# Kernel optimization log

Hardware: AMD Instinct MI355X
Metric: run time of the kernel (lower is better)

The kernel has to match this reference:

```python
import jax, jax.numpy as jnp
import numpy as np

U, I, D, L = 100000, 100000, 64, 50
B, T = 4096, 100


def setup_inputs() -> dict:
    key = jax.random.key(0)
    ks = jax.random.split(key, 12)
    inp = {}
    inp["item_seq"] = jax.random.randint(ks[0], (B, L), 0, I, dtype=jnp.int64 if jax.config.jax_enable_x64 else jnp.int32)
    inp["user_ids"] = jax.random.randint(ks[1], (B,), 0, U, dtype=jnp.int32)
    inp["items_to_predict"] = jax.random.randint(ks[2], (B, T), 0, I, dtype=jnp.int32)
    # parameters (match torch inits: N(0, 1/d) embeddings, xavier gates, zero b2)
    inp["user_emb_table"] = jax.random.normal(ks[3], (U, D), jnp.float32) / D
    inp["item_emb_table"] = jax.random.normal(ks[4], (I, D), jnp.float32) / D
    lin_s = float(np.sqrt(1.0 / D))
    inp["fg_item_W"] = jax.random.uniform(ks[5], (D, D), jnp.float32, -lin_s, lin_s)
    inp["fg_item_b"] = jax.random.uniform(ks[6], (D,), jnp.float32, -lin_s, lin_s)
    inp["fg_user_W"] = jax.random.uniform(ks[7], (D, D), jnp.float32, -lin_s, lin_s)
    inp["fg_user_b"] = jax.random.uniform(ks[8], (D,), jnp.float32, -lin_s, lin_s)
    xg1 = float(np.sqrt(6.0 / (D + 1)))
    xg2 = float(np.sqrt(6.0 / (D + L)))
    inp["instance_gate_item"] = jax.random.uniform(ks[9], (D, 1), jnp.float32, -xg1, xg1)
    inp["instance_gate_user"] = jax.random.uniform(ks[10], (D, L), jnp.float32, -xg2, xg2)
    W2 = jax.random.normal(ks[11], (I, D), jnp.float32) / D
    inp["W2_table"] = W2.at[0].set(0.0)  # padding_idx=0
    inp["b2_table"] = jnp.zeros((I, 1), jnp.float32)
    return inp


def reference(item_seq, user_ids, items_to_predict, user_emb_table, item_emb_table,
              fg_item_W, fg_item_b, fg_user_W, fg_user_b,
              instance_gate_item, instance_gate_user, W2_table, b2_table):
    item_embs = item_emb_table[item_seq]          # [B, L, D]
    user_emb = user_emb_table[user_ids]           # [B, D]
    # feature gating
    gate = jax.nn.sigmoid(item_embs @ fg_item_W + fg_item_b
                          + (user_emb @ fg_user_W + fg_user_b)[:, None, :])
    gated_item = item_embs * gate                 # [B, L, D]
    # instance gating
    instance_score = jax.nn.sigmoid(
        jnp.einsum('bld,d->bl', gated_item, instance_gate_item[:, 0])
        + user_emb @ instance_gate_user)          # [B, L]
    union_out = jnp.sum(gated_item * instance_score[..., None], axis=1)
    union_out = union_out / jnp.sum(instance_score, axis=1, keepdims=True)  # [B, D]
    # scoring (for_pred=False branch)
    w2 = W2_table[items_to_predict]               # [B, T, D]
    b2 = b2_table[items_to_predict][..., 0]       # [B, T]
    res = b2 + jnp.einsum('btd,bd->bt', w2, user_emb)
    res = res + jnp.einsum('btd,bd->bt', w2, union_out)
    # rel_score: sum_l item_embs @ w2^T == (sum_l item_embs) . w2
    res = res + jnp.einsum('bd,btd->bt', item_embs.sum(axis=1), w2)
    return res
```

## Files before the change

### kernel.cpp

```cpp
#include <hip/hip_runtime.h>

#define D_ 64
#define L_ 50
#define B_ 4096
#define T_ 100
#define SP 65
#define RS 72

typedef __attribute__((ext_vector_type(8))) short  short8;
typedef __attribute__((ext_vector_type(4))) float  float4v;
typedef __attribute__((ext_vector_type(4))) unsigned short ushort4v;

__device__ __forceinline__ float sigmoidf_(float x) {
    return 1.0f / (1.0f + __expf(-x));
}
__device__ __forceinline__ unsigned short f2bf(float x) {
    unsigned u = __builtin_bit_cast(unsigned, x);
    return (unsigned short)((u + 0x7fffu + ((u >> 16) & 1u)) >> 16);
}
__device__ __forceinline__ float bf2f(unsigned short s) {
    return __builtin_bit_cast(float, (unsigned)s << 16);
}

__global__ __launch_bounds__(256)
void hgn_fused_kernel(
    const int* __restrict__ item_seq,
    const int* __restrict__ user_ids,
    const int* __restrict__ items_to_predict,
    const float* __restrict__ user_emb_table,
    const float* __restrict__ item_emb_table,
    const float* __restrict__ fg_item_W,
    const float* __restrict__ fg_item_b,
    const float* __restrict__ fg_user_W,
    const float* __restrict__ fg_user_b,
    const float* __restrict__ ig_item,
    const float* __restrict__ ig_user,
    const float* __restrict__ W2,
    const float* __restrict__ b2,
    float* __restrict__ out)
{
    __shared__ unsigned short eb_sh[64 * RS];
    __shared__ unsigned short wbT_sh[64 * RS];
    __shared__ float part_sh[L_ * SP];
    __shared__ __align__(16) float u_sh[D_];
    __shared__ __align__(16) float v_sh[D_];
    __shared__ float gb_sh[D_];
    __shared__ float s_sh[L_];
    __shared__ float esum_sh[D_];
    __shared__ int   idx_sh[L_];

    const int t    = threadIdx.x;
    const int lane = t & 63;
    const int wave = t >> 6;
    const int b    = blockIdx.x;

    if (t < L_) idx_sh[t] = item_seq[b * L_ + t];
    if (t >= 64 && t < 128) {
        const int uid = user_ids[b];
        u_sh[t - 64] = user_emb_table[(size_t)uid * D_ + (t - 64)];
    }
    for (int i = t; i < 14 * RS; i += 256) eb_sh[50 * RS + i] = 0;
    __syncthreads();

    if (wave == 1) {
        float gbv = fg_item_b[lane] + fg_user_b[lane];
#pragma unroll
        for (int k = 0; k < D_; ++k)
            gbv = fmaf(u_sh[k], fg_user_W[k * D_ + lane], gbv);
        gb_sh[lane] = gbv;
    } else {
        const int s = (wave == 0) ? t : (t - 64);
        for (int i = s; i < L_ * 16; i += 192) {
            const int l = i >> 4, qd = i & 15;
            const float4 r = ((const float4*)(item_emb_table + (size_t)idx_sh[l] * D_))[qd];
            ushort4v o = { f2bf(r.x), f2bf(r.y), f2bf(r.z), f2bf(r.w) };
            *(ushort4v*)&eb_sh[l * RS + qd * 4] = o;
        }
        for (int i = s; i < 1024; i += 192) {
            const int k = i >> 4, c4 = (i & 15) * 4;
            const float4 r = ((const float4*)(fg_item_W + k * D_))[i & 15];
            wbT_sh[(c4 + 0) * RS + k] = f2bf(r.x);
            wbT_sh[(c4 + 1) * RS + k] = f2bf(r.y);
            wbT_sh[(c4 + 2) * RS + k] = f2bf(r.z);
            wbT_sh[(c4 + 3) * RS + k] = f2bf(r.w);
        }
    }
    __syncthreads();

    {
        const int m = lane & 15, q = lane >> 4;
        const int arow = 16 * wave + m;
        const short8 a0 = *(const short8*)&eb_sh[arow * RS + q * 8];
        const short8 a1 = *(const short8*)&eb_sh[arow * RS + 32 + q * 8];
#pragma unroll
        for (int n = 0; n < 4; ++n) {
            const int bcol = 16 * n + m;
            const short8 b0 = *(const short8*)&wbT_sh[bcol * RS + q * 8];
            const short8 b1 = *(const short8*)&wbT_sh[bcol * RS + 32 + q * 8];
            float4v acc = {0.f, 0.f, 0.f, 0.f};
            acc = __builtin_amdgcn_mfma_f32_16x16x32_bf16(a0, b0, acc, 0, 0, 0);
            acc = __builtin_amdgcn_mfma_f32_16x16x32_bf16(a1, b1, acc, 0, 0, 0);
#pragma unroll
            for (int r = 0; r < 4; ++r) {
                const int l = 16 * wave + q * 4 + r;
                if (l < L_) part_sh[l * SP + 16 * n + m] = acc[r];
            }
        }
    }
    __syncthreads();

    for (int i = t; i < L_ * D_; i += 256) {
        const int l = i >> 6, d = i & 63;
        const float e = bf2f(eb_sh[l * RS + d]);
        const float gate = sigmoidf_(part_sh[l * SP + d] + gb_sh[d]);
        part_sh[l * SP + d] = e * gate;
    }
    __syncthreads();

    if (wave == 0 && lane < L_) {
        float p0 = 0.f, p1 = 0.f, p2 = 0.f, p3 = 0.f;
#pragma unroll
        for (int d = 0; d < D_; d += 4) {
            p0 = fmaf(part_sh[lane * SP + d + 0], ig_item[d + 0], p0);
            p1 = fmaf(part_sh[lane * SP + d + 1], ig_item[d + 1], p1);
            p2 = fmaf(part_sh[lane * SP + d + 2], ig_item[d + 2], p2);
            p3 = fmaf(part_sh[lane * SP + d + 3], ig_item[d + 3], p3);
            p0 = fmaf(u_sh[d + 0], ig_user[(d + 0) * L_ + lane], p0);
            p1 = fmaf(u_sh[d + 1], ig_user[(d + 1) * L_ + lane], p1);
            p2 = fmaf(u_sh[d + 2], ig_user[(d + 2) * L_ + lane], p2);
            p3 = fmaf(u_sh[d + 3], ig_user[(d + 3) * L_ + lane], p3);
        }
        s_sh[lane] = sigmoidf_((p0 + p1) + (p2 + p3));
    }
    if (wave == 1) {
        float es = 0.f;
#pragma unroll 2
        for (int l = 0; l < L_; ++l) es += bf2f(eb_sh[l * RS + lane]);
        esum_sh[lane] = es;
    }
    __syncthreads();

    if (wave == 0) {
        float a0 = 0.f, a1 = 0.f, ss = 0.f;
        for (int l = 0; l < L_; l += 2) {
            const float sA = s_sh[l], sB = s_sh[l + 1];
            a0 = fmaf(part_sh[l * SP + lane], sA, a0);
            a1 = fmaf(part_sh[(l + 1) * SP + lane], sB, a1);
            ss += sA + sB;
        }
        v_sh[lane] = u_sh[lane] + (a0 + a1) / ss + esum_sh[lane];
    }
    __syncthreads();

    if (t < 2 * T_) {
        const int tt = t >> 1, half = t & 1;
        const int idx = items_to_predict[b * T_ + tt];
        const float* wrow  = W2 + (size_t)idx * D_ + half * 32;
        const float* vhalf = v_sh + half * 32;
        float r0 = 0.f, r1 = 0.f, r2 = 0.f, r3 = 0.f;
#pragma unroll
        for (int kk = 0; kk < 8; ++kk) {
            const float4 w4 = ((const float4*)wrow)[kk];
            const float4 v4 = ((const float4*)vhalf)[kk];
            r0 = fmaf(v4.x, w4.x, r0);
            r1 = fmaf(v4.y, w4.y, r1);
            r2 = fmaf(v4.z, w4.z, r2);
            r3 = fmaf(v4.w, w4.w, r3);
        }
        float r = (r0 + r1) + (r2 + r3);
        r += __shfl_xor(r, 1, 64);
        if (half == 0) out[b * T_ + tt] = r + b2[idx];
    }
}

extern "C" void kernel_launch(void* const* d_in, const int* in_sizes, int n_in,
                              void* d_out, int out_size, void* d_ws, size_t ws_size,
                              hipStream_t stream) {
    const int*   item_seq   = (const int*)d_in[0];
    const int*   user_ids   = (const int*)d_in[1];
    const int*   items_pred = (const int*)d_in[2];
    const float* uet        = (const float*)d_in[3];
    const float* iet        = (const float*)d_in[4];
    const float* fgiW       = (const float*)d_in[5];
    const float* fgib       = (const float*)d_in[6];
    const float* fguW       = (const float*)d_in[7];
    const float* fgub       = (const float*)d_in[8];
    const float* igi        = (const float*)d_in[9];
    const float* igu        = (const float*)d_in[10];
    const float* W2         = (const float*)d_in[11];
    const float* b2t        = (const float*)d_in[12];

    hgn_fused_kernel<<<B_, 256, 0, stream>>>(
        item_seq, user_ids, items_pred, uet, iet,
        fgiW, fgib, fguW, fgub, igi, igu, W2, b2t, (float*)d_out);
}
```

Measured before the change: 169.2 us.

## Precompute bf16 transposed gate weight once and fuse gating into MFMA epilogue

A small pre-kernel now converts fg_item_W to bf16 and transposes it once into workspace. The fused kernel then reads the B operand straight from global/L2 instead of having every block rebuild it in LDS with scattered stores. The sigmoid gating is applied directly in the MFMA epilogue, which removes an LDS pass and a barrier. The instance-score dot product is split across two waves, and the gate-bias and item-sum loops are rebalanced across waves. The costs are an extra kernel launch and global loads of the weight operand inside the matmul, and the zero-fill of the padding rows is dropped.

```diff
diff --git a/kernel.cpp b/kernel.cpp
--- a/kernel.cpp
+++ b/kernel.cpp
@@ -22,14 +22,21 @@
     return __builtin_bit_cast(float, (unsigned)s << 16);
 }
 
-__global__ __launch_bounds__(256)
-void hgn_fused_kernel(
+__global__ __launch_bounds__(256) void hgn_transpose_w(
+    const float* __restrict__ fg_item_W, unsigned short* __restrict__ wbT)
+{
+    const int i = blockIdx.x * 256 + threadIdx.x;
+    const int k = i >> 6, c = i & 63;
+    wbT[c * 64 + k] = f2bf(fg_item_W[i]);
+}
+
+__global__ __launch_bounds__(256) void hgn_fused_kernel(
     const int* __restrict__ item_seq,
     const int* __restrict__ user_ids,
     const int* __restrict__ items_to_predict,
     const float* __restrict__ user_emb_table,
     const float* __restrict__ item_emb_table,
-    const float* __restrict__ fg_item_W,
+    const unsigned short* __restrict__ wbT,
     const float* __restrict__ fg_item_b,
     const float* __restrict__ fg_user_W,
     const float* __restrict__ fg_user_b,
@@ -40,12 +47,12 @@
     float* __restrict__ out)
 {
     __shared__ unsigned short eb_sh[64 * RS];
-    __shared__ unsigned short wbT_sh[64 * RS];
     __shared__ float part_sh[L_ * SP];
     __shared__ __align__(16) float u_sh[D_];
     __shared__ __align__(16) float v_sh[D_];
     __shared__ float gb_sh[D_];
     __shared__ float s_sh[L_];
+    __shared__ float bp_sh[2][64];
     __shared__ float esum_sh[D_];
     __shared__ int   idx_sh[L_];
 
@@ -59,30 +66,24 @@
         const int uid = user_ids[b];
         u_sh[t - 64] = user_emb_table[(size_t)uid * D_ + (t - 64)];
     }
-    for (int i = t; i < 14 * RS; i += 256) eb_sh[50 * RS + i] = 0;
-    __syncthreads();
-
-    if (wave == 1) {
-        float gbv = fg_item_b[lane] + fg_user_b[lane];
-#pragma unroll
-        for (int k = 0; k < D_; ++k)
-            gbv = fmaf(u_sh[k], fg_user_W[k * D_ + lane], gbv);
-        gb_sh[lane] = gbv;
+    __syncthreads();
+
+    if (wave == 3) {
+        float g0 = fg_item_b[lane], g1 = fg_user_b[lane], g2 = 0.f, g3 = 0.f;
+#pragma unroll
+        for (int k = 0; k < D_; k += 4) {
+            g0 = fmaf(u_sh[k + 0], fg_user_W[(k + 0) * D_ + lane], g0);
+            g1 = fmaf(u_sh[k + 1], fg_user_W[(k + 1) * D_ + lane], g1);
+            g2 = fmaf(u_sh[k + 2], fg_user_W[(k + 2) * D_ + lane], g2);
+            g3 = fmaf(u_sh[k + 3], fg_user_W[(k + 3) * D_ + lane], g3);
+        }
+        gb_sh[lane] = (g0 + g1) + (g2 + g3);
     } else {
-        const int s = (wave == 0) ? t : (t - 64);
-        for (int i = s; i < L_ * 16; i += 192) {
+        for (int i = t; i < L_ * 16; i += 192) {
             const int l = i >> 4, qd = i & 15;
             const float4 r = ((const float4*)(item_emb_table + (size_t)idx_sh[l] * D_))[qd];
             ushort4v o = { f2bf(r.x), f2bf(r.y), f2bf(r.z), f2bf(r.w) };
             *(ushort4v*)&eb_sh[l * RS + qd * 4] = o;
-        }
-        for (int i = s; i < 1024; i += 192) {
-            const int k = i >> 4, c4 = (i & 15) * 4;
-            const float4 r = ((const float4*)(fg_item_W + k * D_))[i & 15];
-            wbT_sh[(c4 + 0) * RS + k] = f2bf(r.x);
-            wbT_sh[(c4 + 1) * RS + k] = f2bf(r.y);
-            wbT_sh[(c4 + 2) * RS + k] = f2bf(r.z);
-            wbT_sh[(c4 + 3) * RS + k] = f2bf(r.w);
         }
     }
     __syncthreads();
@@ -94,53 +95,56 @@
         const short8 a1 = *(const short8*)&eb_sh[arow * RS + 32 + q * 8];
 #pragma unroll
         for (int n = 0; n < 4; ++n) {
-            const int bcol = 16 * n + m;
-            const short8 b0 = *(const short8*)&wbT_sh[bcol * RS + q * 8];
-            const short8 b1 = *(const short8*)&wbT_sh[bcol * RS + 32 + q * 8];
+            const int col = 16 * n + m;
+            const short8 b0 = *(const short8*)&wbT[col * 64 + q * 8];
+            const short8 b1 = *(const short8*)&wbT[col * 64 + 32 + q * 8];
             float4v acc = {0.f, 0.f, 0.f, 0.f};
             acc = __builtin_amdgcn_mfma_f32_16x16x32_bf16(a0, b0, acc, 0, 0, 0);
             acc = __builtin_amdgcn_mfma_f32_16x16x32_bf16(a1, b1, acc, 0, 0, 0);
+            const float gbc = gb_sh[col];
 #pragma unroll
             for (int r = 0; r < 4; ++r) {
                 const int l = 16 * wave + q * 4 + r;
-                if (l < L_) part_sh[l * SP + 16 * n + m] = acc[r];
+                if (l < L_) {
+                    const float e = bf2f(eb_sh[l * RS + col]);
+                    part_sh[l * SP + col] = e * sigmoidf_(acc[r] + gbc);
+                }
             }
         }
     }
     __syncthreads();
 
-    for (int i = t; i < L_ * D_; i += 256) {
-        const int l = i >> 6, d = i & 63;
-        const float e = bf2f(eb_sh[l * RS + d]);
-        const float gate = sigmoidf_(part_sh[l * SP + d] + gb_sh[d]);
-        part_sh[l * SP + d] = e * gate;
-    }
-    __syncthreads();
-
-    if (wave == 0 && lane < L_) {
-        float p0 = 0.f, p1 = 0.f, p2 = 0.f, p3 = 0.f;
-#pragma unroll
-        for (int d = 0; d < D_; d += 4) {
-            p0 = fmaf(part_sh[lane * SP + d + 0], ig_item[d + 0], p0);
-            p1 = fmaf(part_sh[lane * SP + d + 1], ig_item[d + 1], p1);
-            p2 = fmaf(part_sh[lane * SP + d + 2], ig_item[d + 2], p2);
-            p3 = fmaf(part_sh[lane * SP + d + 3], ig_item[d + 3], p3);
-            p0 = fmaf(u_sh[d + 0], ig_user[(d + 0) * L_ + lane], p0);
-            p1 = fmaf(u_sh[d + 1], ig_user[(d + 1) * L_ + lane], p1);
-            p2 = fmaf(u_sh[d + 2], ig_user[(d + 2) * L_ + lane], p2);
-            p3 = fmaf(u_sh[d + 3], ig_user[(d + 3) * L_ + lane], p3);
-        }
-        s_sh[lane] = sigmoidf_((p0 + p1) + (p2 + p3));
-    }
-    if (wave == 1) {
-        float es = 0.f;
-#pragma unroll 2
-        for (int l = 0; l < L_; ++l) es += bf2f(eb_sh[l * RS + lane]);
-        esum_sh[lane] = es;
+    if (wave < 2) {
+        if (lane < L_) {
+            const int d0 = 32 * wave;
+            float p0 = 0.f, p1 = 0.f, p2 = 0.f, p3 = 0.f;
+#pragma unroll
+            for (int j = 0; j < 32; j += 4) {
+                const int d = d0 + j;
+                p0 = fmaf(part_sh[lane * SP + d + 0], ig_item[d + 0], p0);
+                p1 = fmaf(part_sh[lane * SP + d + 1], ig_item[d + 1], p1);
+                p2 = fmaf(part_sh[lane * SP + d + 2], ig_item[d + 2], p2);
+                p3 = fmaf(part_sh[lane * SP + d + 3], ig_item[d + 3], p3);
+                p0 = fmaf(u_sh[d + 0], ig_user[(d + 0) * L_ + lane], p0);
+                p1 = fmaf(u_sh[d + 1], ig_user[(d + 1) * L_ + lane], p1);
+                p2 = fmaf(u_sh[d + 2], ig_user[(d + 2) * L_ + lane], p2);
+                p3 = fmaf(u_sh[d + 3], ig_user[(d + 3) * L_ + lane], p3);
+            }
+            bp_sh[wave][lane] = (p0 + p1) + (p2 + p3);
+        }
+    } else if (wave == 2) {
+        float e0 = 0.f, e1 = 0.f;
+#pragma unroll
+        for (int l = 0; l < L_; l += 2) {
+            e0 += bf2f(eb_sh[l * RS + lane]);
+            e1 += bf2f(eb_sh[(l + 1) * RS + lane]);
+        }
+        esum_sh[lane] = e0 + e1;
     }
     __syncthreads();
 
     if (wave == 0) {
+        if (lane < L_) s_sh[lane] = sigmoidf_(bp_sh[0][lane] + bp_sh[1][lane]);
         float a0 = 0.f, a1 = 0.f, ss = 0.f;
         for (int l = 0; l < L_; l += 2) {
             const float sA = s_sh[l], sB = s_sh[l + 1];
@@ -190,7 +194,10 @@
     const float* W2         = (const float*)d_in[11];
     const float* b2t        = (const float*)d_in[12];
 
+    unsigned short* wbT = (unsigned short*)d_ws;
+
+    hgn_transpose_w<<<16, 256, 0, stream>>>(fgiW, wbT);
     hgn_fused_kernel<<<B_, 256, 0, stream>>>(
         item_seq, user_ids, items_pred, uet, iet,
-        fgiW, fgib, fguW, fgub, igi, igu, W2, b2t, (float*)d_out);
-}
+        wbT, fgib, fguW, fgub, igi, igu, W2, b2t, (float*)d_out);
+}
```

Result: faster. 165.3 us (-2.3%).
